# Optimization experiments

Hardware: AMD Instinct MI355X
Metric: run time of the kernel (lower is better)

The kernel has to match this reference:

```python
import jax, jax.numpy as jnp
import numpy as np

K = 4096          # num_embeddings
D = 256           # embedding_dim
BETA = 0.25
DECAY = 0.99
EPS = 1e-05

def setup_inputs() -> dict:
    key = jax.random.key(0)
    k1, k2, k3 = jax.random.split(key, 3)
    N = 65536
    return {
        "z": jax.random.normal(k1, (N, D), dtype=jnp.float32),
        "weight": jax.random.normal(k2, (K, D), dtype=jnp.float32),
        "ema_w": jax.random.normal(k3, (K, D), dtype=jnp.float32),
        "ema_cluster_size": jnp.ones((K,), dtype=jnp.float32),
    }

def reference(z, weight, ema_w, ema_cluster_size):
    # pairwise squared distances: [N, K]
    d = (jnp.sum(z * z, axis=1, keepdims=True)
         + jnp.sum(weight * weight, axis=1)
         - 2.0 * jnp.matmul(z, weight.T))
    idx = jnp.argmin(d, axis=1)                     # [N]
    encodings = jax.nn.one_hot(idx, K, dtype=z.dtype)  # [N, K]

    # EMA codebook update (training branch). In torch the results are re-wrapped
    # into fresh nn.Parameters, which detaches them from the autograd graph.
    def _ema(z_, enc_, ema_w_, cs_):
        cs = cs_ * DECAY + (1.0 - DECAY) * jnp.sum(enc_, axis=0)
        n = jnp.sum(cs)
        cs = (cs + EPS) / (n + K * EPS) * n
        dw = jnp.matmul(enc_.T, z_)                 # [K, D] scatter-add of z by code
        new_ema_w = ema_w_ * DECAY + (1.0 - DECAY) * dw
        new_weight = new_ema_w / cs[:, None]
        return cs, new_ema_w, new_weight
    new_cs, new_ema_w, new_weight = jax.lax.stop_gradient(
        _ema(z, encodings, ema_w, ema_cluster_size))

    z_q = new_weight[idx]                           # [N, D] gather from updated codebook
    loss = (jnp.mean((jax.lax.stop_gradient(z_q) - z) ** 2)
            + BETA * jnp.mean((z_q - jax.lax.stop_gradient(z)) ** 2))
    avg_probs = jnp.mean(encodings, axis=0)
    perplexity = jnp.exp(-jnp.sum(avg_probs * jnp.log(avg_probs + 1e-10)))
    z_q = z + jax.lax.stop_gradient(z_q - z)        # straight-through estimator
    return (z_q, idx[:, None], loss, perplexity, new_cs, new_ema_w, new_weight)
```

## Files before the change

### kernel.cpp

```cpp
#include <hip/hip_runtime.h>
#include <math.h>

#define NPTS 65536
#define DIMD 256
#define KCB  4096
#define MARGIN 2.0f

#define O_ZQ   0
#define O_IDX  16777216
#define O_LOSS 16842752
#define O_PERP 16842753
#define O_CS   16842754
#define O_EMAW 16846850
#define O_W    17895426

#define OFF_WSW   8388608
#define OFF_CCNT  8912896
#define OFF_CIDS  8978432
#define OFF_OFFS  10027008
#define OFF_CUR   10031232
#define OFF_ROWS  10035328
#define OFF_GMIN  10100864
#define OFF_CHOF  10166400

#define CHK 64
#define MAXCHUNKS 5120

#define RING 6
#define PFD  4

typedef __attribute__((ext_vector_type(8))) short short8;
typedef __attribute__((ext_vector_type(4))) float f32x4;

__device__ __forceinline__ unsigned short f2bf(float f) {
    unsigned u = __float_as_uint(f);
    return (unsigned short)((u + 0x7FFF + ((u >> 16) & 1)) >> 16);
}
__device__ __forceinline__ unsigned encf(float f) {
    unsigned u = __float_as_uint(f);
    return (u >> 31) ? ~u : (u | 0x80000000u);
}
__device__ __forceinline__ float decf(unsigned e) {
    unsigned u = (e & 0x80000000u) ? (e & 0x7fffffffu) : ~e;
    return __uint_as_float(u);
}

__global__ void k_prepz(const float* __restrict__ src, unsigned* __restrict__ dst,
                        float* __restrict__ ss) {
    int l   = threadIdx.x & 63;
    int row = blockIdx.x * 4 + (threadIdx.x >> 6);
    float4 v = ((const float4*)(src + (size_t)row * DIMD))[l];
    uint2 pk = make_uint2(f2bf(v.x) | (f2bf(v.y) << 16),
                          f2bf(v.z) | (f2bf(v.w) << 16));
    ((uint2*)dst)[(size_t)row * 64 + l] = pk;
    float s = v.x*v.x + v.y*v.y + v.z*v.z + v.w*v.w;
    #pragma unroll
    for (int off = 32; off; off >>= 1) s += __shfl_down(s, off);
    if (l == 0) ss[row] = s;
}

__global__ void k_prepw(const float* __restrict__ src, unsigned* __restrict__ dst,
                        float* __restrict__ ss) {
    int l   = threadIdx.x & 63;
    int row = blockIdx.x * 4 + (threadIdx.x >> 6);
    float4 v = ((const float4*)(src + (size_t)row * DIMD))[l];
    uint2 pk = make_uint2(f2bf(v.x) | (f2bf(v.y) << 16),
                          f2bf(v.z) | (f2bf(v.w) << 16));
    int g = row >> 4, n16 = row & 15;
    int c = l >> 3, q = (l >> 1) & 3, half = l & 1;
    ((uint2*)dst)[g * 1024 + c * 128 + (q * 16 + n16) * 2 + half] = pk;
    float s = v.x*v.x + v.y*v.y + v.z*v.z + v.w*v.w;
    #pragma unroll
    for (int off = 32; off; off >>= 1) s += __shfl_down(s, off);
    if (l == 0) ss[row] = s;
}

__launch_bounds__(256, 2)
__global__ void k_pass0(const unsigned* __restrict__ zbf,
                        const uint4* __restrict__ wsw4,
                        const float* __restrict__ wwg,
                        unsigned* __restrict__ gmin) {
    __shared__ __align__(16) char smem[RING * 8192];
    __shared__ float lds_ww[2048];
    const int t = threadIdx.x, wv = t >> 6, l = t & 63;
    const int q = l >> 4, n16 = l & 15;
    const int rb    = blockIdx.x >> 1;
    const int half  = blockIdx.x & 1;
    const int row0  = rb * 256 + wv * 64;
    const int g0    = half * 128;
    const int ph0   = (blockIdx.x * 37) & 127;

    union U { uint4 u; short8 s; } afr[4][8];
    #pragma unroll
    for (int s = 0; s < 4; ++s) {
        const char* zb = (const char*)zbf + ((size_t)(row0 + s * 16 + n16) << 9) + q * 16;
        #pragma unroll
        for (int c = 0; c < 8; ++c) afr[s][c].u = *(const uint4*)(zb + c * 64);
    }

    auto stage = [&](int buf, int g) {
        const int ga = (ph0 + g) & 127;
        const uint4* srcb = wsw4 + (size_t)(g0 + ga) * 512;
        #pragma unroll
        for (int j = 0; j < 2; ++j) {
            int rrow = j * 4 + wv;
            __builtin_amdgcn_global_load_lds(
                (const __attribute__((address_space(1))) unsigned*)(srcb + rrow * 64 + l),
                (__attribute__((address_space(3))) unsigned*)(&smem[buf * 8192 + rrow * 1024]),
                16, 0, 0);
        }
    };

    for (int i = t; i < 2048; i += 256) lds_ww[i] = wwg[g0 * 16 + i];
    #pragma unroll
    for (int g = 0; g < PFD; ++g) stage(g, g);
    __syncthreads();

    float minv[16];
    #pragma unroll
    for (int i = 0; i < 16; ++i) minv[i] = 3.0e38f;

    int buf = 0, sbuf = PFD;
    #pragma unroll 1
    for (int g = 0; g < 128 - PFD; ++g) {
        stage(sbuf, g + PFD);
        sbuf = (sbuf == RING - 1) ? 0 : sbuf + 1;
        asm volatile("s_waitcnt vmcnt(8)" ::: "memory");
        __builtin_amdgcn_s_barrier();
        const char* sbase = smem + buf * 8192;
        buf = (buf == RING - 1) ? 0 : buf + 1;
        const int ga = (ph0 + g) & 127;
        f32x4 acc[4];
        #pragma unroll
        for (int s = 0; s < 4; ++s) acc[s] = (f32x4){0.f, 0.f, 0.f, 0.f};
        __builtin_amdgcn_s_setprio(1);
        #pragma unroll
        for (int c = 0; c < 8; ++c) {
            U bf; bf.u = *(const uint4*)(sbase + c * 1024 + (l << 4));
            #pragma unroll
            for (int s = 0; s < 4; ++s)
                acc[s] = __builtin_amdgcn_mfma_f32_16x16x32_bf16(afr[s][c].s, bf.s, acc[s], 0, 0, 0);
        }
        __builtin_amdgcn_s_setprio(0);
        float wwv = lds_ww[ga * 16 + n16];
        #pragma unroll
        for (int s = 0; s < 4; ++s)
            #pragma unroll
            for (int r = 0; r < 4; ++r)
                minv[s*4+r] = fminf(minv[s*4+r], fmaf(-2.f, acc[s][r], wwv));
    }
    #pragma unroll 1
    for (int g = 128 - PFD; g < 128; ++g) {
        asm volatile("s_waitcnt vmcnt(0)" ::: "memory");
        __builtin_amdgcn_s_barrier();
        const char* sbase = smem + buf * 8192;
        buf = (buf == RING - 1) ? 0 : buf + 1;
        const int ga = (ph0 + g) & 127;
        f32x4 acc[4];
        #pragma unroll
        for (int s = 0; s < 4; ++s) acc[s] = (f32x4){0.f, 0.f, 0.f, 0.f};
        #pragma unroll
        for (int c = 0; c < 8; ++c) {
            U bf; bf.u = *(const uint4*)(sbase + c * 1024 + (l << 4));
            #pragma unroll
            for (int s = 0; s < 4; ++s)
                acc[s] = __builtin_amdgcn_mfma_f32_16x16x32_bf16(afr[s][c].s, bf.s, acc[s], 0, 0, 0);
        }
        float wwv = lds_ww[ga * 16 + n16];
        #pragma unroll
        for (int s = 0; s < 4; ++s)
            #pragma unroll
            for (int r = 0; r < 4; ++r)
                minv[s*4+r] = fminf(minv[s*4+r], fmaf(-2.f, acc[s][r], wwv));
    }

    #pragma unroll
    for (int i = 0; i < 16; ++i) {
        float m = minv[i];
        #pragma unroll
        for (int msk = 1; msk < 16; msk <<= 1) m = fminf(m, __shfl_xor(m, msk));
        if (n16 == 0)
            atomicMin(&gmin[row0 + (i >> 2) * 16 + q * 4 + (i & 3)], encf(m));
    }
}

__launch_bounds__(256, 2)
__global__ void k_pass1(const unsigned* __restrict__ zbf,
                        const uint4* __restrict__ wsw4,
                        const float* __restrict__ wwg,
                        const unsigned* __restrict__ gmin,
                        int* __restrict__ ccnt,
                        int* __restrict__ cids) {
    __shared__ __align__(16) char smem[RING * 8192];
    __shared__ float lds_ww[2048];
    __shared__ int   lds_cnt[256];
    __shared__ short lds_cid[256 * 16];
    const int t = threadIdx.x, wv = t >> 6, l = t & 63;
    const int q = l >> 4, n16 = l & 15;
    const int rb    = blockIdx.x >> 1;
    const int half  = blockIdx.x & 1;
    const int row0  = rb * 256 + wv * 64;
    const int g0    = half * 128;
    const int ph0   = (blockIdx.x * 37) & 127;

    union U { uint4 u; short8 s; } afr[4][8];
    #pragma unroll
    for (int s = 0; s < 4; ++s) {
        const char* zb = (const char*)zbf + ((size_t)(row0 + s * 16 + n16) << 9) + q * 16;
        #pragma unroll
        for (int c = 0; c < 8; ++c) afr[s][c].u = *(const uint4*)(zb + c * 64);
    }

    auto stage = [&](int buf, int g) {
        const int ga = (ph0 + g) & 127;
        const uint4* srcb = wsw4 + (size_t)(g0 + ga) * 512;
        #pragma unroll
        for (int j = 0; j < 2; ++j) {
            int rrow = j * 4 + wv;
            __builtin_amdgcn_global_load_lds(
                (const __attribute__((address_space(1))) unsigned*)(srcb + rrow * 64 + l),
                (__attribute__((address_space(3))) unsigned*)(&smem[buf * 8192 + rrow * 1024]),
                16, 0, 0);
        }
    };

    float thr[16];
    #pragma unroll
    for (int i = 0; i < 16; ++i)
        thr[i] = decf(gmin[row0 + (i >> 2) * 16 + q * 4 + (i & 3)]) + MARGIN;

    for (int i = t; i < 2048; i += 256) lds_ww[i] = wwg[g0 * 16 + i];
    lds_cnt[t] = 0;
    #pragma unroll
    for (int g = 0; g < PFD; ++g) stage(g, g);
    __syncthreads();

    int buf = 0, sbuf = PFD;
    #pragma unroll 1
    for (int g = 0; g < 128; ++g) {
        if (g < 128 - PFD) {
            stage(sbuf, g + PFD);
            sbuf = (sbuf == RING - 1) ? 0 : sbuf + 1;
            asm volatile("s_waitcnt vmcnt(8)" ::: "memory");
        } else {
            asm volatile("s_waitcnt vmcnt(0)" ::: "memory");
        }
        __builtin_amdgcn_s_barrier();
        const char* sbase = smem + buf * 8192;
        buf = (buf == RING - 1) ? 0 : buf + 1;
        const int ga = (ph0 + g) & 127;
        f32x4 acc[4];
        #pragma unroll
        for (int s = 0; s < 4; ++s) acc[s] = (f32x4){0.f, 0.f, 0.f, 0.f};
        __builtin_amdgcn_s_setprio(1);
        #pragma unroll
        for (int c = 0; c < 8; ++c) {
            U bf; bf.u = *(const uint4*)(sbase + c * 1024 + (l << 4));
            #pragma unroll
            for (int s = 0; s < 4; ++s)
                acc[s] = __builtin_amdgcn_mfma_f32_16x16x32_bf16(afr[s][c].s, bf.s, acc[s], 0, 0, 0);
        }
        __builtin_amdgcn_s_setprio(0);
        const int gg = g0 + ga;
        float wwv = lds_ww[ga * 16 + n16];
        #pragma unroll
        for (int s = 0; s < 4; ++s)
            #pragma unroll
            for (int r = 0; r < 4; ++r) {
                float core = fmaf(-2.f, acc[s][r], wwv);
                if (core <= thr[s*4+r]) {
                    int rl = wv * 64 + s * 16 + q * 4 + r;
                    int p = atomicAdd(&lds_cnt[rl], 1);
                    if (p < 16) lds_cid[rl * 16 + p] = (short)(gg * 16 + n16);
                }
            }
    }

    __syncthreads();
    int n = lds_cnt[t];
    if (n > 0) {
        int rg = rb * 256 + t;
        int base = atomicAdd(&ccnt[rg], n);
        int m = n > 16 ? 16 : n;
        for (int j = 0; j < m; ++j) {
            int p = base + j;
            if (p < 16) cids[rg * 16 + p] = (int)lds_cid[t * 16 + j];
        }
    }
}

__global__ void k_refine(const float* __restrict__ z,
                         const float* __restrict__ w,
                         const float* __restrict__ zz,
                         const float* __restrict__ wwg,
                         const int* __restrict__ ccnt,
                         const int* __restrict__ cids,
                         float* __restrict__ counts,
                         int*   __restrict__ idxi,
                         float* __restrict__ idxf) {
    int l   = threadIdx.x & 63;
    int row = blockIdx.x * 4 + (threadIdx.x >> 6);
    int n = ccnt[row]; if (n > 16) n = 16;
    float4 zv = ((const float4*)(z + (size_t)row * DIMD))[l];
    float zzv = zz[row];
    float bd = 3.0e38f; int bi = 0x7fffffff;
    for (int j = 0; j < n; ++j) {
        int k = cids[row * 16 + j];
        float4 wv = ((const float4*)(w + (size_t)k * DIMD))[l];
        float s = zv.x*wv.x + zv.y*wv.y + zv.z*wv.z + zv.w*wv.w;
        #pragma unroll
        for (int off = 32; off; off >>= 1) s += __shfl_xor(s, off);
        float d = (zzv + wwg[k]) - 2.0f * s;
        if (d < bd || (d == bd && k < bi)) { bd = d; bi = k; }
    }
    if (l == 0) {
        idxi[row] = bi;
        idxf[row] = (float)bi;
        atomicAdd(&counts[bi], 1.0f);
    }
}

__global__ void k_offsets(const float* __restrict__ counts,
                          int* __restrict__ offs, int* __restrict__ cursor,
                          int* __restrict__ choffs) {
    __shared__ int sc[1024];
    int t = threadIdx.x;
    int c[4]; int s = 0;
    #pragma unroll
    for (int i = 0; i < 4; ++i) { c[i] = (int)counts[t * 4 + i]; s += c[i]; }
    sc[t] = s;
    __syncthreads();
    for (int d = 1; d < 1024; d <<= 1) {
        int v = (t >= d) ? sc[t - d] : 0;
        __syncthreads();
        sc[t] += v;
        __syncthreads();
    }
    int o = sc[t] - s;
    #pragma unroll
    for (int i = 0; i < 4; ++i) { offs[t*4+i] = o; cursor[t*4+i] = o; o += c[i]; }
    if (t == 1023) offs[4096] = sc[1023];
    __syncthreads();

    int ch[4]; int s2 = 0;
    #pragma unroll
    for (int i = 0; i < 4; ++i) { ch[i] = (c[i] + CHK - 1) / CHK; s2 += ch[i]; }
    sc[t] = s2;
    __syncthreads();
    for (int d = 1; d < 1024; d <<= 1) {
        int v = (t >= d) ? sc[t - d] : 0;
        __syncthreads();
        sc[t] += v;
        __syncthreads();
    }
    int o2 = sc[t] - s2;
    #pragma unroll
    for (int i = 0; i < 4; ++i) { choffs[t*4+i] = o2; o2 += ch[i]; }
    if (t == 1023) choffs[4096] = sc[1023];
}

__global__ void k_fill(const int* __restrict__ idxi, int* __restrict__ cursor,
                       int* __restrict__ rows) {
    int r = blockIdx.x * 256 + threadIdx.x;
    int k = idxi[r];
    int pos = atomicAdd(&cursor[k], 1);
    rows[pos] = r;
}

__global__ void k_dw(const float* __restrict__ z, const int* __restrict__ offs,
                     const int* __restrict__ choffs, const int* __restrict__ rows,
                     float* __restrict__ dw) {
    __shared__ float4 part[4][64];
    int b = blockIdx.x;
    if (b >= choffs[KCB]) return;
    int lo = 0, hi = KCB;
    while (hi - lo > 1) { int mid = (lo + hi) >> 1; if (choffs[mid] <= b) lo = mid; else hi = mid; }
    int k  = lo;
    int ci = b - choffs[k];
    int o0 = offs[k] + ci * CHK;
    int o1 = offs[k + 1]; if (o1 > o0 + CHK) o1 = o0 + CHK;
    int l = threadIdx.x & 63, j = threadIdx.x >> 6;
    float4 a = make_float4(0.f, 0.f, 0.f, 0.f);
    for (int i = o0 + j; i < o1; i += 4) {
        int r = rows[i];
        float4 v = ((const float4*)(z + (size_t)r * DIMD))[l];
        a.x += v.x; a.y += v.y; a.z += v.z; a.w += v.w;
    }
    part[j][l] = a;
    __syncthreads();
    if (j == 0) {
        float4 bb = part[0][l], c = part[1][l], d = part[2][l], e = part[3][l];
        a = make_float4(bb.x+c.x+d.x+e.x, bb.y+c.y+d.y+e.y,
                        bb.z+c.z+d.z+e.z, bb.w+c.w+d.w+e.w);
        float* p = dw + (size_t)k * DIMD + l * 4;
        if (choffs[k + 1] - choffs[k] == 1) {
            *(float4*)p = a;
        } else {
            atomicAdd(p + 0, a.x); atomicAdd(p + 1, a.y);
            atomicAdd(p + 2, a.z); atomicAdd(p + 3, a.w);
        }
    }
}

__global__ void k_cs(const float* __restrict__ ema_cs,
                     float* __restrict__ cs_io,
                     float* __restrict__ perp) {
    __shared__ float2 red[16];
    int t = threadIdx.x;
    float csd[4];
    float nl = 0.f, el = 0.f;
    #pragma unroll
    for (int i = 0; i < 4; ++i) {
        int k = t * 4 + i;
        float c  = cs_io[k];
        float cd = ema_cs[k] * 0.99f + 0.01f * c;
        csd[i] = cd;
        nl += cd;
        float p = c * (1.0f / 65536.0f);
        el += p * logf(p + 1e-10f);
    }
    #pragma unroll
    for (int off = 32; off; off >>= 1) { nl += __shfl_down(nl, off); el += __shfl_down(el, off); }
    if ((t & 63) == 0) red[t >> 6] = make_float2(nl, el);
    __syncthreads();
    if (t == 0) {
        float n = 0.f, e = 0.f;
        for (int i = 0; i < 16; ++i) { n += red[i].x; e += red[i].y; }
        red[0] = make_float2(n, e);
        perp[0] = expf(-e);
    }
    __syncthreads();
    float n = red[0].x;
    float scale = n / (n + 4096.0f * 1e-5f);
    #pragma unroll
    for (int i = 0; i < 4; ++i)
        cs_io[t * 4 + i] = (csd[i] + 1e-5f) * scale;
}

__global__ void k_emaw(const float* __restrict__ ema_w,
                       const float* __restrict__ cs,
                       float* __restrict__ emaw_io,
                       float* __restrict__ wout) {
    int i = (blockIdx.x * 256 + threadIdx.x) * 4;
    int k = i >> 8;
    float4 dv = *(const float4*)(emaw_io + i);
    float4 ev = *(const float4*)(ema_w + i);
    float c = cs[k];
    float4 ne;
    ne.x = ev.x * 0.99f + 0.01f * dv.x;
    ne.y = ev.y * 0.99f + 0.01f * dv.y;
    ne.z = ev.z * 0.99f + 0.01f * dv.z;
    ne.w = ev.w * 0.99f + 0.01f * dv.w;
    *(float4*)(emaw_io + i) = ne;
    float4 nw = make_float4(ne.x / c, ne.y / c, ne.z / c, ne.w / c);
    *(float4*)(wout + i) = nw;
}

__global__ void k_zq(const float* __restrict__ z,
                     const float* __restrict__ wnew,
                     const int* __restrict__ idxi,
                     float* __restrict__ zq,
                     float* __restrict__ sqacc) {
    __shared__ float red[4];
    int i = (blockIdx.x * 256 + threadIdx.x) * 4;
    int n = i >> 8;
    int d = i & 255;
    int k = idxi[n];
    float4 wv = *(const float4*)(wnew + (k << 8) + d);
    float4 zv = *(const float4*)(z + i);
    float4 o;
    o.x = zv.x + (wv.x - zv.x);
    o.y = zv.y + (wv.y - zv.y);
    o.z = zv.z + (wv.z - zv.z);
    o.w = zv.w + (wv.w - zv.w);
    *(float4*)(zq + i) = o;
    float dx = wv.x - zv.x, dy = wv.y - zv.y, dz = wv.z - zv.z, dw_ = wv.w - zv.w;
    float s = dx*dx + dy*dy + dz*dz + dw_*dw_;
    #pragma unroll
    for (int off = 32; off; off >>= 1) s += __shfl_down(s, off);
    int lane = threadIdx.x & 63;
    if (lane == 0) red[threadIdx.x >> 6] = s;
    __syncthreads();
    if (threadIdx.x == 0)
        atomicAdd(&sqacc[blockIdx.x & 255], red[0] + red[1] + red[2] + red[3]);
}

__global__ void k_final(const float* __restrict__ sqacc, float* __restrict__ loss) {
    __shared__ float red[4];
    int t = threadIdx.x;
    float s = sqacc[t];
    #pragma unroll
    for (int off = 32; off; off >>= 1) s += __shfl_down(s, off);
    if ((t & 63) == 0) red[t >> 6] = s;
    __syncthreads();
    if (t == 0)
        loss[0] = 1.25f * (red[0] + red[1] + red[2] + red[3]) * (1.0f / 16777216.0f);
}

extern "C" void kernel_launch(void* const* d_in, const int* in_sizes, int n_in,
                              void* d_out, int out_size, void* d_ws, size_t ws_size,
                              hipStream_t stream) {
    const float* z      = (const float*)d_in[0];
    const float* weight = (const float*)d_in[1];
    const float* ema_w  = (const float*)d_in[2];
    const float* ema_cs = (const float*)d_in[3];
    float* out = (float*)d_out;
    float* ws  = (float*)d_ws;

    float* scal = ws + 4096;
    int*   idxi = (int*)(ws + 8192);

    unsigned* zbf    = (unsigned*)(out + O_ZQ);
    uint4*    wsw4   = (uint4*)(out + O_ZQ + OFF_WSW);
    int*      ccnt   = (int*)(out + O_ZQ + OFF_CCNT);
    int*      cids   = (int*)(out + O_ZQ + OFF_CIDS);
    int*      offs   = (int*)(out + O_ZQ + OFF_OFFS);
    int*      cursor = (int*)(out + O_ZQ + OFF_CUR);
    int*      rows   = (int*)(out + O_ZQ + OFF_ROWS);
    unsigned* gmin   = (unsigned*)(out + O_ZQ + OFF_GMIN);
    int*      choffs = (int*)(out + O_ZQ + OFF_CHOF);
    float*    zz     = out + O_EMAW;
    float*    wwg    = out + O_EMAW + 65536;

    hipMemsetAsync(scal,       0,    256 * 4, stream);
    hipMemsetAsync(out + O_CS, 0,    (size_t)KCB * 4, stream);
    hipMemsetAsync(ccnt,       0,    (size_t)NPTS * 4, stream);
    hipMemsetAsync(gmin,       0xFF, (size_t)NPTS * 4, stream);

    k_prepz  <<<NPTS / 4, 256, 0, stream>>>(z, zbf, zz);
    k_prepw  <<<KCB  / 4, 256, 0, stream>>>(weight, (unsigned*)wsw4, wwg);
    k_pass0  <<<512, 256, 0, stream>>>(zbf, wsw4, wwg, gmin);
    k_pass1  <<<512, 256, 0, stream>>>(zbf, wsw4, wwg, gmin, ccnt, cids);
    k_refine <<<NPTS / 4, 256, 0, stream>>>(z, weight, zz, wwg, ccnt, cids,
                                            out + O_CS, idxi, out + O_IDX);
    hipMemsetAsync(out + O_EMAW, 0, (size_t)KCB * DIMD * 4, stream);
    k_offsets<<<1, 1024, 0, stream>>>(out + O_CS, offs, cursor, choffs);
    k_fill   <<<NPTS / 256, 256, 0, stream>>>(idxi, cursor, rows);
    k_cs     <<<1, 1024, 0, stream>>>(ema_cs, out + O_CS, out + O_PERP);
    k_dw     <<<MAXCHUNKS, 256, 0, stream>>>(z, offs, choffs, rows, out + O_EMAW);
    k_emaw   <<<(KCB * DIMD) / 1024, 256, 0, stream>>>(ema_w, out + O_CS,
                                                       out + O_EMAW, out + O_W);
    k_zq     <<<(NPTS * DIMD) / 1024, 256, 0, stream>>>(z, out + O_W, idxi,
                                                        out + O_ZQ, scal);
    k_final  <<<1, 256, 0, stream>>>(scal, out + O_LOSS);
}
```

Measured before the change: 513.2 us.

## Prune second distance pass using per-block minima to recompute only candidate code blocks

Pass 0 now also records, for each row, the minimum approximate distance within each 256-code block. New kernels select the rows whose block minimum falls within the margin of the global minimum and bucket them per block into padded 64-row tiles. Pass 1 then recomputes bf16 distances only for those (row, block) tiles rather than for every row against the full codebook. The cost is extra bmin writes, two small selection kernels, and a pass 1 that reads weights directly from global memory with global atomics. It also changes the block phase stride in pass 0.

```diff
diff --git a/kernel.cpp b/kernel.cpp
--- a/kernel.cpp
+++ b/kernel.cpp
@@ -22,9 +22,13 @@
 #define OFF_ROWS  10035328
 #define OFF_GMIN  10100864
 #define OFF_CHOF  10166400
+#define OFF_BMIN  10240000
+#define OFF_RL    11288576
+#define OFF_TPRE  12338176
 
 #define CHK 64
 #define MAXCHUNKS 5120
+#define PADL 65600
 
 #define RING 6
 #define PFD  4
@@ -79,7 +83,8 @@
 __global__ void k_pass0(const unsigned* __restrict__ zbf,
                         const uint4* __restrict__ wsw4,
                         const float* __restrict__ wwg,
-                        unsigned* __restrict__ gmin) {
+                        unsigned* __restrict__ gmin,
+                        float* __restrict__ bmin) {
     __shared__ __align__(16) char smem[RING * 8192];
     __shared__ float lds_ww[2048];
     const int t = threadIdx.x, wv = t >> 6, l = t & 63;
@@ -88,7 +93,7 @@
     const int half  = blockIdx.x & 1;
     const int row0  = rb * 256 + wv * 64;
     const int g0    = half * 128;
-    const int ph0   = (blockIdx.x * 37) & 127;
+    const int ph0   = (blockIdx.x * 48) & 127;
 
     union U { uint4 u; short8 s; } afr[4][8];
     #pragma unroll
@@ -116,124 +121,9 @@
     for (int g = 0; g < PFD; ++g) stage(g, g);
     __syncthreads();
 
-    float minv[16];
-    #pragma unroll
-    for (int i = 0; i < 16; ++i) minv[i] = 3.0e38f;
-
-    int buf = 0, sbuf = PFD;
-    #pragma unroll 1
-    for (int g = 0; g < 128 - PFD; ++g) {
-        stage(sbuf, g + PFD);
-        sbuf = (sbuf == RING - 1) ? 0 : sbuf + 1;
-        asm volatile("s_waitcnt vmcnt(8)" ::: "memory");
-        __builtin_amdgcn_s_barrier();
-        const char* sbase = smem + buf * 8192;
-        buf = (buf == RING - 1) ? 0 : buf + 1;
-        const int ga = (ph0 + g) & 127;
-        f32x4 acc[4];
-        #pragma unroll
-        for (int s = 0; s < 4; ++s) acc[s] = (f32x4){0.f, 0.f, 0.f, 0.f};
-        __builtin_amdgcn_s_setprio(1);
-        #pragma unroll
-        for (int c = 0; c < 8; ++c) {
-            U bf; bf.u = *(const uint4*)(sbase + c * 1024 + (l << 4));
-            #pragma unroll
-            for (int s = 0; s < 4; ++s)
-                acc[s] = __builtin_amdgcn_mfma_f32_16x16x32_bf16(afr[s][c].s, bf.s, acc[s], 0, 0, 0);
-        }
-        __builtin_amdgcn_s_setprio(0);
-        float wwv = lds_ww[ga * 16 + n16];
-        #pragma unroll
-        for (int s = 0; s < 4; ++s)
-            #pragma unroll
-            for (int r = 0; r < 4; ++r)
-                minv[s*4+r] = fminf(minv[s*4+r], fmaf(-2.f, acc[s][r], wwv));
-    }
-    #pragma unroll 1
-    for (int g = 128 - PFD; g < 128; ++g) {
-        asm volatile("s_waitcnt vmcnt(0)" ::: "memory");
-        __builtin_amdgcn_s_barrier();
-        const char* sbase = smem + buf * 8192;
-        buf = (buf == RING - 1) ? 0 : buf + 1;
-        const int ga = (ph0 + g) & 127;
-        f32x4 acc[4];
-        #pragma unroll
-        for (int s = 0; s < 4; ++s) acc[s] = (f32x4){0.f, 0.f, 0.f, 0.f};
-        #pragma unroll
-        for (int c = 0; c < 8; ++c) {
-            U bf; bf.u = *(const uint4*)(sbase + c * 1024 + (l << 4));
-            #pragma unroll
-            for (int s = 0; s < 4; ++s)
-                acc[s] = __builtin_amdgcn_mfma_f32_16x16x32_bf16(afr[s][c].s, bf.s, acc[s], 0, 0, 0);
-        }
-        float wwv = lds_ww[ga * 16 + n16];
-        #pragma unroll
-        for (int s = 0; s < 4; ++s)
-            #pragma unroll
-            for (int r = 0; r < 4; ++r)
-                minv[s*4+r] = fminf(minv[s*4+r], fmaf(-2.f, acc[s][r], wwv));
-    }
-
-    #pragma unroll
-    for (int i = 0; i < 16; ++i) {
-        float m = minv[i];
-        #pragma unroll
-        for (int msk = 1; msk < 16; msk <<= 1) m = fminf(m, __shfl_xor(m, msk));
-        if (n16 == 0)
-            atomicMin(&gmin[row0 + (i >> 2) * 16 + q * 4 + (i & 3)], encf(m));
-    }
-}
-
-__launch_bounds__(256, 2)
-__global__ void k_pass1(const unsigned* __restrict__ zbf,
-                        const uint4* __restrict__ wsw4,
-                        const float* __restrict__ wwg,
-                        const unsigned* __restrict__ gmin,
-                        int* __restrict__ ccnt,
-                        int* __restrict__ cids) {
-    __shared__ __align__(16) char smem[RING * 8192];
-    __shared__ float lds_ww[2048];
-    __shared__ int   lds_cnt[256];
-    __shared__ short lds_cid[256 * 16];
-    const int t = threadIdx.x, wv = t >> 6, l = t & 63;
-    const int q = l >> 4, n16 = l & 15;
-    const int rb    = blockIdx.x >> 1;
-    const int half  = blockIdx.x & 1;
-    const int row0  = rb * 256 + wv * 64;
-    const int g0    = half * 128;
-    const int ph0   = (blockIdx.x * 37) & 127;
-
-    union U { uint4 u; short8 s; } afr[4][8];
-    #pragma unroll
-    for (int s = 0; s < 4; ++s) {
-        const char* zb = (const char*)zbf + ((size_t)(row0 + s * 16 + n16) << 9) + q * 16;
-        #pragma unroll
-        for (int c = 0; c < 8; ++c) afr[s][c].u = *(const uint4*)(zb + c * 64);
-    }
-
-    auto stage = [&](int buf, int g) {
-        const int ga = (ph0 + g) & 127;
-        const uint4* srcb = wsw4 + (size_t)(g0 + ga) * 512;
-        #pragma unroll
-        for (int j = 0; j < 2; ++j) {
-            int rrow = j * 4 + wv;
-            __builtin_amdgcn_global_load_lds(
-                (const __attribute__((address_space(1))) unsigned*)(srcb + rrow * 64 + l),
-                (__attribute__((address_space(3))) unsigned*)(&smem[buf * 8192 + rrow * 1024]),
-                16, 0, 0);
-        }
-    };
-
-    float thr[16];
-    #pragma unroll
-    for (int i = 0; i < 16; ++i)
-        thr[i] = decf(gmin[row0 + (i >> 2) * 16 + q * 4 + (i & 3)]) + MARGIN;
-
-    for (int i = t; i < 2048; i += 256) lds_ww[i] = wwg[g0 * 16 + i];
-    lds_cnt[t] = 0;
-    #pragma unroll
-    for (int g = 0; g < PFD; ++g) stage(g, g);
-    __syncthreads();
+    float minv[16], bm[16];
+    #pragma unroll
+    for (int i = 0; i < 16; ++i) { minv[i] = 3.0e38f; bm[i] = 3.0e38f; }
 
     int buf = 0, sbuf = PFD;
     #pragma unroll 1
@@ -261,30 +151,137 @@
                 acc[s] = __builtin_amdgcn_mfma_f32_16x16x32_bf16(afr[s][c].s, bf.s, acc[s], 0, 0, 0);
         }
         __builtin_amdgcn_s_setprio(0);
-        const int gg = g0 + ga;
         float wwv = lds_ww[ga * 16 + n16];
         #pragma unroll
         for (int s = 0; s < 4; ++s)
             #pragma unroll
-            for (int r = 0; r < 4; ++r) {
-                float core = fmaf(-2.f, acc[s][r], wwv);
-                if (core <= thr[s*4+r]) {
-                    int rl = wv * 64 + s * 16 + q * 4 + r;
-                    int p = atomicAdd(&lds_cnt[rl], 1);
-                    if (p < 16) lds_cid[rl * 16 + p] = (short)(gg * 16 + n16);
+            for (int r = 0; r < 4; ++r)
+                bm[s*4+r] = fminf(bm[s*4+r], fmaf(-2.f, acc[s][r], wwv));
+        if ((g & 15) == 15) {
+            const int blk = (g0 + ((ph0 + (g & ~15)) & 127)) >> 4;
+            #pragma unroll
+            for (int i = 0; i < 16; ++i) {
+                float m = bm[i];
+                minv[i] = fminf(minv[i], m);
+                #pragma unroll
+                for (int msk = 1; msk < 16; msk <<= 1) m = fminf(m, __shfl_xor(m, msk));
+                if (n16 == 0)
+                    bmin[(size_t)(row0 + (i >> 2) * 16 + q * 4 + (i & 3)) * 16 + blk] = m;
+                bm[i] = 3.0e38f;
+            }
+        }
+    }
+
+    #pragma unroll
+    for (int i = 0; i < 16; ++i) {
+        float m = minv[i];
+        #pragma unroll
+        for (int msk = 1; msk < 16; msk <<= 1) m = fminf(m, __shfl_xor(m, msk));
+        if (n16 == 0)
+            atomicMin(&gmin[row0 + (i >> 2) * 16 + q * 4 + (i & 3)], encf(m));
+    }
+}
+
+__global__ void k_bsel(const unsigned* __restrict__ gmin,
+                       const float* __restrict__ bmin,
+                       int* __restrict__ bcnt, int* __restrict__ rlist) {
+    __shared__ int lcnt[16], lbase[16], lcur[16];
+    int t = threadIdx.x;
+    if (t < 16) { lcnt[t] = 0; lcur[t] = 0; }
+    __syncthreads();
+    int row = blockIdx.x * 256 + t;
+    float thr = decf(gmin[row]) + MARGIN;
+    const float* bm = bmin + (size_t)row * 16;
+    unsigned qual = 0;
+    #pragma unroll
+    for (int b = 0; b < 16; ++b)
+        if (bm[b] <= thr) { qual |= (1u << b); atomicAdd(&lcnt[b], 1); }
+    __syncthreads();
+    if (t < 16) lbase[t] = atomicAdd(&bcnt[t], lcnt[t]);
+    __syncthreads();
+    #pragma unroll
+    for (int b = 0; b < 16; ++b)
+        if (qual & (1u << b)) {
+            int p = atomicAdd(&lcur[b], 1);
+            rlist[b * PADL + lbase[b] + p] = row;
+        }
+}
+
+__global__ void k_btile(const int* __restrict__ bcnt, int* __restrict__ rlist,
+                        int* __restrict__ tpre) {
+    __shared__ int tb[16];
+    int t = threadIdx.x;
+    if (t < 16) tb[t] = (bcnt[t] + 63) >> 6;
+    __syncthreads();
+    int b = t >> 4, j = t & 15;
+    int n = bcnt[b], e = tb[b] * 64;
+    for (int i = n + j; i < e; i += 16) rlist[b * PADL + i] = -1;
+    if (t == 0) {
+        int s = 0;
+        for (int b2 = 0; b2 < 16; ++b2) { tpre[b2] = s; s += tb[b2]; }
+        tpre[16] = s;
+    }
+}
+
+__launch_bounds__(256, 2)
+__global__ void k_pass1(const unsigned* __restrict__ zbf,
+                        const uint4* __restrict__ wsw4,
+                        const float* __restrict__ wwg,
+                        const unsigned* __restrict__ gmin,
+                        const int* __restrict__ tpre,
+                        const int* __restrict__ rlist,
+                        int* __restrict__ ccnt,
+                        int* __restrict__ cids) {
+    const int t = threadIdx.x, wv = t >> 6, l = t & 63;
+    const int q = l >> 4, n16 = l & 15;
+    const int ntiles = tpre[16];
+    for (int tile = blockIdx.x * 4 + wv; tile < ntiles; tile += 2048) {
+        int b = 0;
+        while (b < 15 && tpre[b + 1] <= tile) ++b;
+        const int* rl = rlist + b * PADL + (tile - tpre[b]) * 64;
+
+        union U { uint4 u; short8 s; } afr[4][8];
+        #pragma unroll
+        for (int s = 0; s < 4; ++s) {
+            int r = rl[s * 16 + n16];
+            int rr = r < 0 ? 0 : r;
+            const char* zb = (const char*)zbf + ((size_t)rr << 9) + q * 16;
+            #pragma unroll
+            for (int c = 0; c < 8; ++c) afr[s][c].u = *(const uint4*)(zb + c * 64);
+        }
+        float thr[16];
+        #pragma unroll
+        for (int i = 0; i < 16; ++i) {
+            int r = rl[(i >> 2) * 16 + q * 4 + (i & 3)];
+            thr[i] = (r < 0) ? -3.0e38f : decf(gmin[r]) + MARGIN;
+        }
+
+        #pragma unroll 2
+        for (int g = 0; g < 16; ++g) {
+            const int gg = b * 16 + g;
+            const uint4* wp = wsw4 + (size_t)gg * 512 + l;
+            f32x4 acc[4];
+            #pragma unroll
+            for (int s = 0; s < 4; ++s) acc[s] = (f32x4){0.f, 0.f, 0.f, 0.f};
+            #pragma unroll
+            for (int c = 0; c < 8; ++c) {
+                U bf; bf.u = wp[c * 64];
+                #pragma unroll
+                for (int s = 0; s < 4; ++s)
+                    acc[s] = __builtin_amdgcn_mfma_f32_16x16x32_bf16(afr[s][c].s, bf.s, acc[s], 0, 0, 0);
+            }
+            float wwv = wwg[gg * 16 + n16];
+            #pragma unroll
+            for (int s = 0; s < 4; ++s)
+                #pragma unroll
+                for (int r = 0; r < 4; ++r) {
+                    float core = fmaf(-2.f, acc[s][r], wwv);
+                    if (core <= thr[s*4+r]) {
+                        int row = rl[s * 16 + q * 4 + r];
+                        int pos = atomicAdd(&ccnt[row], 1);
+                        if (pos < 16) cids[row * 16 + pos] = gg * 16 + n16;
+                    }
                 }
-            }
-    }
-
-    __syncthreads();
-    int n = lds_cnt[t];
-    if (n > 0) {
-        int rg = rb * 256 + t;
-        int base = atomicAdd(&ccnt[rg], n);
-        int m = n > 16 ? 16 : n;
-        for (int j = 0; j < m; ++j) {
-            int p = base + j;
-            if (p < 16) cids[rg * 16 + p] = (int)lds_cid[t * 16 + j];
         }
     }
 }
@@ -507,6 +504,7 @@
     float* out = (float*)d_out;
     float* ws  = (float*)d_ws;
 
+    int*   bcnt = (int*)ws;
     float* scal = ws + 4096;
     int*   idxi = (int*)(ws + 8192);
 
@@ -519,9 +517,13 @@
     int*      rows   = (int*)(out + O_ZQ + OFF_ROWS);
     unsigned* gmin   = (unsigned*)(out + O_ZQ + OFF_GMIN);
     int*      choffs = (int*)(out + O_ZQ + OFF_CHOF);
+    float*    bmin   = out + O_ZQ + OFF_BMIN;
+    int*      rlist  = (int*)(out + O_ZQ + OFF_RL);
+    int*      tpre   = (int*)(out + O_ZQ + OFF_TPRE);
     float*    zz     = out + O_EMAW;
     float*    wwg    = out + O_EMAW + 65536;
 
+    hipMemsetAsync(bcnt,       0,    16 * 4, stream);
     hipMemsetAsync(scal,       0,    256 * 4, stream);
     hipMemsetAsync(out + O_CS, 0,    (size_t)KCB * 4, stream);
     hipMemsetAsync(ccnt,       0,    (size_t)NPTS * 4, stream);
@@ -529,8 +531,11 @@
 
     k_prepz  <<<NPTS / 4, 256, 0, stream>>>(z, zbf, zz);
     k_prepw  <<<KCB  / 4, 256, 0, stream>>>(weight, (unsigned*)wsw4, wwg);
-    k_pass0  <<<512, 256, 0, stream>>>(zbf, wsw4, wwg, gmin);
-    k_pass1  <<<512, 256, 0, stream>>>(zbf, wsw4, wwg, gmin, ccnt, cids);
+    k_pass0  <<<512, 256, 0, stream>>>(zbf, wsw4, wwg, gmin, bmin);
+    k_bsel   <<<NPTS / 256, 256, 0, stream>>>(gmin, bmin, bcnt, rlist);
+    k_btile  <<<1, 256, 0, stream>>>(bcnt, rlist, tpre);
+    k_pass1  <<<512, 256, 0, stream>>>(zbf, wsw4, wwg, gmin, tpre, rlist,
+                                       ccnt, cids);
     k_refine <<<NPTS / 4, 256, 0, stream>>>(z, weight, zz, wwg, ccnt, cids,
                                             out + O_CS, idxi, out + O_IDX);
     hipMemsetAsync(out + O_EMAW, 0, (size_t)KCB * DIMD * 4, stream);
```

Result: faster. 494.9 us (-3.6%).
